# Kernel tuning notes

Hardware: AMD Instinct MI355X
Metric: run time of the kernel (lower is better)

Reference implementation:

```python
import jax, jax.numpy as jnp
import numpy as np

B = 2
T = 1024
D_MODEL = 1024
EXPAND = 2
D_INNER = D_MODEL * EXPAND  # 2048
D_STATE = 16
D_CONV = 4
DT_RANK = 64  # ceil(1024/16)


def setup_inputs() -> dict:
    key = jax.random.key(0)
    ks = jax.random.split(key, 9)
    s = 0.02
    x = jax.random.normal(ks[0], (B, T, D_MODEL), jnp.float32)
    in_proj_w = jax.random.normal(ks[1], (2 * D_INNER, D_MODEL), jnp.float32) * s
    conv_w = jax.random.normal(ks[2], (D_INNER, 1, D_CONV), jnp.float32) * 0.1
    conv_b = jax.random.normal(ks[3], (D_INNER,), jnp.float32) * 0.01
    x_proj_w = jax.random.normal(ks[4], (DT_RANK + 2 * D_STATE, D_INNER), jnp.float32) * s
    dt_proj_w = jax.random.normal(ks[5], (D_INNER, DT_RANK), jnp.float32) * s
    dt_proj_b = jax.random.uniform(ks[6], (D_INNER,), jnp.float32, -4.0, -2.0)
    A_log = jnp.log(jnp.tile(jnp.arange(1, D_STATE + 1, dtype=jnp.float32), (D_INNER, 1)))
    D_param = jnp.ones((D_INNER,), jnp.float32)
    out_proj_w = jax.random.normal(ks[7], (D_MODEL, D_INNER), jnp.float32) * s
    return {"x": x, "in_proj_w": in_proj_w, "conv_w": conv_w, "conv_b": conv_b,
            "x_proj_w": x_proj_w, "dt_proj_w": dt_proj_w, "dt_proj_b": dt_proj_b,
            "A_log": A_log, "D_param": D_param, "out_proj_w": out_proj_w}


def reference(x, in_proj_w, conv_w, conv_b, x_proj_w, dt_proj_w, dt_proj_b,
              A_log, D_param, out_proj_w):
    Bsz, Tlen, _ = x.shape
    # input projection -> (B,T,2*d_inner); split into x-branch and gate z
    xz = jnp.einsum('btd,ed->bte', x, in_proj_w)
    xs, z = jnp.split(xz, 2, axis=-1)
    # causal depthwise conv1d: torch pads both sides by d_conv-1 then slices [:T],
    # equivalent to left-pad d_conv-1
    xc = jnp.swapaxes(xs, 1, 2)  # (B, d_inner, T)
    xc = jax.lax.conv_general_dilated(xc, conv_w, window_strides=(1,),
                                      padding=[(D_CONV - 1, 0)],
                                      feature_group_count=D_INNER)
    xc = xc + conv_b[None, :, None]
    xs = jax.nn.silu(jnp.swapaxes(xc, 1, 2))  # (B,T,d_inner)
    A = -jnp.exp(A_log)  # (d_inner, d_state)
    x_dbl = jnp.einsum('bti,ei->bte', xs, x_proj_w)
    dt, Bv, Cv = jnp.split(x_dbl, [DT_RANK, DT_RANK + D_STATE], axis=-1)
    dt = jax.nn.softplus(jnp.einsum('btr,ir->bti', dt, dt_proj_w) + dt_proj_b)
    # selective scan: h_t = exp(dt_t*A)*h_{t-1} + (dt_t*x_t)*B_t ; y_t = <h_t, C_t>
    def step(h, inp):
        dt_t, B_t, C_t, x_t = inp  # (B,Di),(B,Ds),(B,Ds),(B,Di)
        dA = jnp.exp(dt_t[:, :, None] * A[None])        # (B,Di,Ds)
        h = dA * h + (dt_t * x_t)[:, :, None] * B_t[:, None, :]
        y_t = jnp.einsum('bds,bs->bd', h, C_t)
        return h, y_t
    tm = lambda a: jnp.swapaxes(a, 0, 1)  # time-major
    h0 = jnp.zeros((Bsz, D_INNER, D_STATE), x.dtype)
    _, ys = jax.lax.scan(step, h0, (tm(dt), tm(Bv), tm(Cv), tm(xs)))
    y = jnp.swapaxes(ys, 0, 1) + xs * D_param  # (B,T,d_inner)
    y = y * jax.nn.silu(z)
    return jnp.einsum('bti,di->btd', y, out_proj_w)
```

## Files before the change

kernel.cpp:

```cpp
#include <hip/hip_runtime.h>
#include <hip/hip_bf16.h>
#include <math.h>

#define B_SZ 2
#define T_LEN 1024
#define DMODEL 1024
#define DINNER 2048
#define DSTATE 16
#define DCONV 4
#define DTRANK 64
#define MTOK (B_SZ * T_LEN)

#define NC 32
#define CLEN (T_LEN / NC)
#define NCH (B_SZ * DINNER)
#define NSTATES (NCH * DSTATE)

#define XPK 8
#define XPKC (DINNER / XPK)

typedef __bf16 bf16x4 __attribute__((ext_vector_type(4)));
typedef __bf16 bf16x8 __attribute__((ext_vector_type(8)));
typedef float  f32x4  __attribute__((ext_vector_type(4)));

__device__ __forceinline__ float sigmoid_f(float v) { return 1.f / (1.f + __expf(-v)); }

__global__ __launch_bounds__(256) void convert4(const float* __restrict__ x,
                                                const float* __restrict__ w_in,
                                                const float* __restrict__ w_out,
                                                const float* __restrict__ w_xp,
                                                __bf16* __restrict__ xb,
                                                __bf16* __restrict__ wb_in,
                                                __bf16* __restrict__ wb_out,
                                                __bf16* __restrict__ wxp,
                                                float* __restrict__ xdbl)
{
    const int gi = blockIdx.x * blockDim.x + threadIdx.x;
    if (gi >= 1073152) {
        const int o = gi - 1073152;
        float4 z = make_float4(0.f, 0.f, 0.f, 0.f);
        reinterpret_cast<float4*>(xdbl)[2 * o]     = z;
        reinterpret_cast<float4*>(xdbl)[2 * o + 1] = z;
        return;
    }
    const float* src; __bf16* dst; int o;
    if (gi < 262144)       { src = x;     dst = xb;     o = gi; }
    else if (gi < 786432)  { src = w_in;  dst = wb_in;  o = gi - 262144; }
    else if (gi < 1048576) { src = w_out; dst = wb_out; o = gi - 786432; }
    else                   { src = w_xp;  dst = wxp;    o = gi - 1048576; }
    float4 a = reinterpret_cast<const float4*>(src)[2 * o];
    float4 b = reinterpret_cast<const float4*>(src)[2 * o + 1];
    bf16x8 v = {(__bf16)a.x, (__bf16)a.y, (__bf16)a.z, (__bf16)a.w,
                (__bf16)b.x, (__bf16)b.y, (__bf16)b.z, (__bf16)b.w};
    reinterpret_cast<bf16x8*>(dst)[o] = v;
}

template<int BN, typename CT>
__global__ __launch_bounds__(256) void mfma_gemm_bf16(const __bf16* __restrict__ A, int lda,
                                                      const __bf16* __restrict__ Bm, int ldb,
                                                      CT* __restrict__ C, int ldc, int K)
{
    constexpr int NF = BN / 32;
    constexpr int BCALLS = BN / 32;
    __shared__ __align__(16) __bf16 As[128 * 64];
    __shared__ __align__(16) __bf16 Bs[BN * 64];
    const int tid  = threadIdx.x;
    const int lane = tid & 63;
    const int w    = tid >> 6;
    const int wr   = w >> 1, wc = w & 1;
    const int m0   = blockIdx.y * 128, n0 = blockIdx.x * BN;

    f32x4 acc[4][NF];
    #pragma unroll
    for (int i = 0; i < 4; ++i)
        #pragma unroll
        for (int j = 0; j < NF; ++j) {
            f32x4 z = {0.f, 0.f, 0.f, 0.f};
            acc[i][j] = z;
        }

    const int fr = lane & 15;
    const int kq = (lane >> 4) * 8;

    for (int k0 = 0; k0 < K; k0 += 64) {
        #pragma unroll
        for (int c = 0; c < 4; ++c) {
            const int idx = c * 256 + tid;
            const int row = idx >> 3;
            const int kc  = (idx & 7) * 8;
            __builtin_amdgcn_global_load_lds(
                (const __attribute__((address_space(1))) unsigned int*)(A + (size_t)(m0 + row) * lda + k0 + kc),
                (__attribute__((address_space(3))) unsigned int*)(As + idx * 8),
                16, 0, 0);
        }
        #pragma unroll
        for (int c = 0; c < BCALLS; ++c) {
            const int idx = c * 256 + tid;
            const int row = idx >> 3;
            const int kc  = (idx & 7) * 8;
            __builtin_amdgcn_global_load_lds(
                (const __attribute__((address_space(1))) unsigned int*)(Bm + (size_t)(n0 + row) * ldb + k0 + kc),
                (__attribute__((address_space(3))) unsigned int*)(Bs + idx * 8),
                16, 0, 0);
        }
        __syncthreads();

        bf16x8 af[4][2], bfr[NF][2];
        #pragma unroll
        for (int i = 0; i < 4; ++i) {
            const __bf16* pa = As + (wr * 64 + i * 16 + fr) * 64 + kq;
            af[i][0] = *reinterpret_cast<const bf16x8*>(pa);
            af[i][1] = *reinterpret_cast<const bf16x8*>(pa + 32);
        }
        #pragma unroll
        for (int j = 0; j < NF; ++j) {
            const __bf16* pb = Bs + (wc * (BN / 2) + j * 16 + fr) * 64 + kq;
            bfr[j][0] = *reinterpret_cast<const bf16x8*>(pb);
            bfr[j][1] = *reinterpret_cast<const bf16x8*>(pb + 32);
        }
        #pragma unroll
        for (int i = 0; i < 4; ++i)
            #pragma unroll
            for (int j = 0; j < NF; ++j) {
                acc[i][j] = __builtin_amdgcn_mfma_f32_16x16x32_bf16(af[i][0], bfr[j][0], acc[i][j], 0, 0, 0);
                acc[i][j] = __builtin_amdgcn_mfma_f32_16x16x32_bf16(af[i][1], bfr[j][1], acc[i][j], 0, 0, 0);
            }
        __syncthreads();
    }

    const int crow = (lane >> 4) * 4;
    const int ccol = lane & 15;
    #pragma unroll
    for (int i = 0; i < 4; ++i)
        #pragma unroll
        for (int j = 0; j < NF; ++j) {
            CT* cp = C + (size_t)(m0 + wr * 64 + i * 16 + crow) * ldc
                       + n0 + wc * (BN / 2) + j * 16 + ccol;
            cp[0 * (size_t)ldc] = (CT)acc[i][j][0];
            cp[1 * (size_t)ldc] = (CT)acc[i][j][1];
            cp[2 * (size_t)ldc] = (CT)acc[i][j][2];
            cp[3 * (size_t)ldc] = (CT)acc[i][j][3];
        }
}

__global__ __launch_bounds__(256) void mfma_xproj(const __bf16* __restrict__ A,
                                                  const __bf16* __restrict__ Bm,
                                                  float* __restrict__ xdbl)
{
    __shared__ __align__(16) __bf16 As[128 * 64];
    __shared__ __align__(16) __bf16 Bs[32 * 64];
    const int tid  = threadIdx.x;
    const int lane = tid & 63;
    const int w    = tid >> 6;
    const int wr   = w >> 1, wc = w & 1;
    const int m0   = blockIdx.y * 128, n0 = blockIdx.x * 32;
    const int kbeg = blockIdx.z * XPKC;

    f32x4 acc[4];
    #pragma unroll
    for (int i = 0; i < 4; ++i) { f32x4 z = {0.f, 0.f, 0.f, 0.f}; acc[i] = z; }

    const int fr = lane & 15;
    const int kq = (lane >> 4) * 8;

    for (int k0 = kbeg; k0 < kbeg + XPKC; k0 += 64) {
        #pragma unroll
        for (int c = 0; c < 4; ++c) {
            const int idx = c * 256 + tid;
            const int row = idx >> 3;
            const int kc  = (idx & 7) * 8;
            __builtin_amdgcn_global_load_lds(
                (const __attribute__((address_space(1))) unsigned int*)(A + (size_t)(m0 + row) * DINNER + k0 + kc),
                (__attribute__((address_space(3))) unsigned int*)(As + idx * 8),
                16, 0, 0);
        }
        {
            const int row = tid >> 3;
            const int kc  = (tid & 7) * 8;
            __builtin_amdgcn_global_load_lds(
                (const __attribute__((address_space(1))) unsigned int*)(Bm + (size_t)(n0 + row) * DINNER + k0 + kc),
                (__attribute__((address_space(3))) unsigned int*)(Bs + tid * 8),
                16, 0, 0);
        }
        __syncthreads();

        bf16x8 af[4][2], bfr[2];
        #pragma unroll
        for (int i = 0; i < 4; ++i) {
            const __bf16* pa = As + (wr * 64 + i * 16 + fr) * 64 + kq;
            af[i][0] = *reinterpret_cast<const bf16x8*>(pa);
            af[i][1] = *reinterpret_cast<const bf16x8*>(pa + 32);
        }
        {
            const __bf16* pb = Bs + (wc * 16 + fr) * 64 + kq;
            bfr[0] = *reinterpret_cast<const bf16x8*>(pb);
            bfr[1] = *reinterpret_cast<const bf16x8*>(pb + 32);
        }
        #pragma unroll
        for (int i = 0; i < 4; ++i) {
            acc[i] = __builtin_amdgcn_mfma_f32_16x16x32_bf16(af[i][0], bfr[0], acc[i], 0, 0, 0);
            acc[i] = __builtin_amdgcn_mfma_f32_16x16x32_bf16(af[i][1], bfr[1], acc[i], 0, 0, 0);
        }
        __syncthreads();
    }

    const int crow = (lane >> 4) * 4;
    const int ccol = lane & 15;
    const int n = n0 + wc * 16 + ccol;
    #pragma unroll
    for (int i = 0; i < 4; ++i) {
        const int m = m0 + wr * 64 + i * 16 + crow;
        unsafeAtomicAdd(&xdbl[(size_t)(m + 0) * 96 + n], acc[i][0]);
        unsafeAtomicAdd(&xdbl[(size_t)(m + 1) * 96 + n], acc[i][1]);
        unsafeAtomicAdd(&xdbl[(size_t)(m + 2) * 96 + n], acc[i][2]);
        unsafeAtomicAdd(&xdbl[(size_t)(m + 3) * 96 + n], acc[i][3]);
    }
}

__global__ __launch_bounds__(256) void mfma_dtproj(const float* __restrict__ xdbl,
                                                   const float* __restrict__ dtw,
                                                   const float* __restrict__ dtbias,
                                                   __bf16* __restrict__ dtb)
{
    __shared__ __align__(16) __bf16 As0[128 * 64];
    __shared__ __align__(16) __bf16 Bs0[128 * 64];
    const int tid  = threadIdx.x;
    const int lane = tid & 63;
    const int w    = tid >> 6;
    const int wr   = w >> 1, wc = w & 1;
    const int m0 = (blockIdx.x >> 4) * 128;
    const int n0 = (blockIdx.x & 15) * 128;

    #pragma unroll
    for (int c = 0; c < 8; ++c) {
        const int idx = c * 256 + tid;
        const int row = idx >> 4;
        const int c4  = (idx & 15) * 4;
        float4 va = *reinterpret_cast<const float4*>(&xdbl[(size_t)(m0 + row) * 96 + c4]);
        bf16x4 ba = {(__bf16)va.x, (__bf16)va.y, (__bf16)va.z, (__bf16)va.w};
        *reinterpret_cast<bf16x4*>(&As0[row * 64 + c4]) = ba;
        float4 vb = *reinterpret_cast<const float4*>(&dtw[(size_t)(n0 + row) * DTRANK + c4]);
        bf16x4 bb = {(__bf16)vb.x, (__bf16)vb.y, (__bf16)vb.z, (__bf16)vb.w};
        *reinterpret_cast<bf16x4*>(&Bs0[row * 64 + c4]) = bb;
    }
    __syncthreads();

    const int fr = lane & 15;
    const int kq = (lane >> 4) * 8;
    f32x4 acc[4][4];
    #pragma unroll
    for (int i = 0; i < 4; ++i)
        #pragma unroll
        for (int j = 0; j < 4; ++j) {
            f32x4 z = {0.f, 0.f, 0.f, 0.f};
            acc[i][j] = z;
        }
    bf16x8 af[4][2], bfr[4][2];
    #pragma unroll
    for (int i = 0; i < 4; ++i) {
        const __bf16* pa = As0 + (wr * 64 + i * 16 + fr) * 64 + kq;
        af[i][0] = *reinterpret_cast<const bf16x8*>(pa);
        af[i][1] = *reinterpret_cast<const bf16x8*>(pa + 32);
    }
    #pragma unroll
    for (int j = 0; j < 4; ++j) {
        const __bf16* pb = Bs0 + (wc * 64 + j * 16 + fr) * 64 + kq;
        bfr[j][0] = *reinterpret_cast<const bf16x8*>(pb);
        bfr[j][1] = *reinterpret_cast<const bf16x8*>(pb + 32);
    }
    #pragma unroll
    for (int i = 0; i < 4; ++i)
        #pragma unroll
        for (int j = 0; j < 4; ++j) {
            acc[i][j] = __builtin_amdgcn_mfma_f32_16x16x32_bf16(af[i][0], bfr[j][0], acc[i][j], 0, 0, 0);
            acc[i][j] = __builtin_amdgcn_mfma_f32_16x16x32_bf16(af[i][1], bfr[j][1], acc[i][j], 0, 0, 0);
        }

    const int crow = (lane >> 4) * 4;
    const int ccol = lane & 15;
    #pragma unroll
    for (int i = 0; i < 4; ++i)
        #pragma unroll
        for (int j = 0; j < 4; ++j) {
            const int m = m0 + wr * 64 + i * 16 + crow;
            const int n = n0 + wc * 64 + j * 16 + ccol;
            const float bn = dtbias[n];
            #pragma unroll
            for (int r = 0; r < 4; ++r) {
                float v = acc[i][j][r] + bn;
                v = (v > 20.f) ? v : log1pf(__expf(v));
                dtb[(size_t)(m + r) * DINNER + n] = (__bf16)v;
            }
        }
}

__global__ __launch_bounds__(256) void conv_silu_v8(const __bf16* __restrict__ xzb,
                                                    const float* __restrict__ cw,
                                                    const float* __restrict__ cb,
                                                    __bf16* __restrict__ xsb)
{
    const int gid = blockIdx.x * blockDim.x + threadIdx.x;
    const int dg  = gid & (DINNER / 8 - 1);
    const int m   = gid >> 8;
    const int t   = m & (T_LEN - 1);
    const int d0  = dg * 8;

    float acc[8];
    {
        float4 b0 = *reinterpret_cast<const float4*>(&cb[d0]);
        float4 b1 = *reinterpret_cast<const float4*>(&cb[d0 + 4]);
        acc[0] = b0.x; acc[1] = b0.y; acc[2] = b0.z; acc[3] = b0.w;
        acc[4] = b1.x; acc[5] = b1.y; acc[6] = b1.z; acc[7] = b1.w;
    }
    float4 wv[8];
    #pragma unroll
    for (int c = 0; c < 8; ++c)
        wv[c] = *reinterpret_cast<const float4*>(&cw[(d0 + c) * DCONV]);

    #pragma unroll
    for (int j = 0; j < DCONV; ++j) {
        const int tt = t - (DCONV - 1) + j;
        if (tt >= 0) {
            bf16x8 v = *reinterpret_cast<const bf16x8*>(
                &xzb[(size_t)(m - (DCONV - 1) + j) * (2 * DINNER) + d0]);
            acc[0] = fmaf((float)v[0], (&wv[0].x)[j], acc[0]);
            acc[1] = fmaf((float)v[1], (&wv[1].x)[j], acc[1]);
            acc[2] = fmaf((float)v[2], (&wv[2].x)[j], acc[2]);
            acc[3] = fmaf((float)v[3], (&wv[3].x)[j], acc[3]);
            acc[4] = fmaf((float)v[4], (&wv[4].x)[j], acc[4]);
            acc[5] = fmaf((float)v[5], (&wv[5].x)[j], acc[5]);
            acc[6] = fmaf((float)v[6], (&wv[6].x)[j], acc[6]);
            acc[7] = fmaf((float)v[7], (&wv[7].x)[j], acc[7]);
        }
    }
    bf16x8 o;
    #pragma unroll
    for (int c = 0; c < 8; ++c) {
        float s = acc[c] * sigmoid_f(acc[c]);
        o[c] = (__bf16)s;
    }
    *reinterpret_cast<bf16x8*>(&xsb[(size_t)m * DINNER + d0]) = o;
}

__global__ __launch_bounds__(256) void scan_pass1(const __bf16* __restrict__ dtb,
                                                  const __bf16* __restrict__ xsb,
                                                  const float* __restrict__ xdbl,
                                                  const float* __restrict__ A_log,
                                                  float* __restrict__ Pb,
                                                  float* __restrict__ Bb)
{
    __shared__ float sB[CLEN][16];
    const int tid = threadIdx.x;
    const int g   = blockIdx.x * 256 + tid;
    const int c   = blockIdx.y;
    const int b   = g >> 11;
    const int d   = g & (DINNER - 1);
    const int m0  = b * T_LEN + c * CLEN;

    if (tid < CLEN * 4) {
        int t = tid >> 2, s4 = (tid & 3) * 4;
        *reinterpret_cast<float4*>(&sB[t][s4]) =
            *reinterpret_cast<const float4*>(&xdbl[(size_t)(m0 + t) * 96 + DTRANK + s4]);
    }
    __syncthreads();

    float a[DSTATE], h[DSTATE];
    #pragma unroll
    for (int s4 = 0; s4 < DSTATE; s4 += 4) {
        float4 v = *reinterpret_cast<const float4*>(&A_log[d * DSTATE + s4]);
        a[s4 + 0] = -__expf(v.x); a[s4 + 1] = -__expf(v.y);
        a[s4 + 2] = -__expf(v.z); a[s4 + 3] = -__expf(v.w);
        h[s4 + 0] = 0.f; h[s4 + 1] = 0.f; h[s4 + 2] = 0.f; h[s4 + 3] = 0.f;
    }

    float sumdt = 0.f;
    float dtc = (float)dtb[(size_t)m0 * DINNER + d];
    float xc  = (float)xsb[(size_t)m0 * DINNER + d];
    for (int t = 0; t < CLEN; ++t) {
        float dtn = 0.f, xn = 0.f;
        if (t + 1 < CLEN) {
            dtn = (float)dtb[(size_t)(m0 + t + 1) * DINNER + d];
            xn  = (float)xsb[(size_t)(m0 + t + 1) * DINNER + d];
        }
        sumdt += dtc;
        const float u = dtc * xc;
        #pragma unroll
        for (int s = 0; s < DSTATE; ++s) {
            const float dA = __expf(dtc * a[s]);
            h[s] = fmaf(dA, h[s], u * sB[t][s]);
        }
        dtc = dtn; xc = xn;
    }

    float* pp = Pb + ((size_t)c * NCH + g) * DSTATE;
    float* bp = Bb + ((size_t)c * NCH + g) * DSTATE;
    #pragma unroll
    for (int s4 = 0; s4 < DSTATE; s4 += 4) {
        float4 pv = {__expf(a[s4] * sumdt), __expf(a[s4 + 1] * sumdt),
                     __expf(a[s4 + 2] * sumdt), __expf(a[s4 + 3] * sumdt)};
        *reinterpret_cast<float4*>(pp + s4) = pv;
        float4 hv = {h[s4], h[s4 + 1], h[s4 + 2], h[s4 + 3]};
        *reinterpret_cast<float4*>(bp + s4) = hv;
    }
}

__global__ __launch_bounds__(256) void scan_pass2(const float* __restrict__ Pb,
                                                  float* __restrict__ Bb)
{
    const int idx = blockIdx.x * blockDim.x + threadIdx.x;
    float h = 0.f;
    #pragma unroll
    for (int c = 0; c < NC; ++c) {
        const size_t o = (size_t)c * NSTATES + idx;
        const float P  = Pb[o];
        const float Bv = Bb[o];
        Bb[o] = h;
        h = fmaf(P, h, Bv);
    }
}

__global__ __launch_bounds__(256) void scan_pass3(const __bf16* __restrict__ dtb,
                                                  const __bf16* __restrict__ xsb,
                                                  const float* __restrict__ xdbl,
                                                  const float* __restrict__ Hs,
                                                  const float* __restrict__ A_log,
                                                  const float* __restrict__ Dp,
                                                  const __bf16* __restrict__ xzb,
                                                  __bf16* __restrict__ yMb)
{
    __shared__ float sBC[CLEN][32];
    const int tid = threadIdx.x;
    const int g   = blockIdx.x * 256 + tid;
    const int c   = blockIdx.y;
    const int b   = g >> 11;
    const int d   = g & (DINNER - 1);
    const int m0  = b * T_LEN + c * CLEN;

    {
        int t = tid >> 3, col = (tid & 7) * 4;
        if (t < CLEN)
            *reinterpret_cast<float4*>(&sBC[t][col]) =
                *reinterpret_cast<const float4*>(&xdbl[(size_t)(m0 + t) * 96 + DTRANK + col]);
    }
    __syncthreads();

    float a[DSTATE], h[DSTATE];
    #pragma unroll
    for (int s4 = 0; s4 < DSTATE; s4 += 4) {
        float4 v = *reinterpret_cast<const float4*>(&A_log[d * DSTATE + s4]);
        a[s4 + 0] = -__expf(v.x); a[s4 + 1] = -__expf(v.y);
        a[s4 + 2] = -__expf(v.z); a[s4 + 3] = -__expf(v.w);
        float4 hv = *reinterpret_cast<const float4*>(
            Hs + ((size_t)c * NCH + g) * DSTATE + s4);
        h[s4 + 0] = hv.x; h[s4 + 1] = hv.y; h[s4 + 2] = hv.z; h[s4 + 3] = hv.w;
    }
    const float Dv = Dp[d];

    float dtc = (float)dtb[(size_t)m0 * DINNER + d];
    float xc  = (float)xsb[(size_t)m0 * DINNER + d];
    float zc  = (float)xzb[(size_t)m0 * (2 * DINNER) + DINNER + d];
    for (int t = 0; t < CLEN; ++t) {
        float dtn = 0.f, xn = 0.f, zn = 0.f;
        if (t + 1 < CLEN) {
            dtn = (float)dtb[(size_t)(m0 + t + 1) * DINNER + d];
            xn  = (float)xsb[(size_t)(m0 + t + 1) * DINNER + d];
            zn  = (float)xzb[(size_t)(m0 + t + 1) * (2 * DINNER) + DINNER + d];
        }
        const float u = dtc * xc;
        float y0 = 0.f, y1 = 0.f, y2 = 0.f, y3 = 0.f;
        #pragma unroll
        for (int s = 0; s < DSTATE; s += 4) {
            float dA0 = __expf(dtc * a[s + 0]);
            float dA1 = __expf(dtc * a[s + 1]);
            float dA2 = __expf(dtc * a[s + 2]);
            float dA3 = __expf(dtc * a[s + 3]);
            h[s + 0] = fmaf(dA0, h[s + 0], u * sBC[t][s + 0]);
            h[s + 1] = fmaf(dA1, h[s + 1], u * sBC[t][s + 1]);
            h[s + 2] = fmaf(dA2, h[s + 2], u * sBC[t][s + 2]);
            h[s + 3] = fmaf(dA3, h[s + 3], u * sBC[t][s + 3]);
            y0 = fmaf(h[s + 0], sBC[t][16 + s + 0], y0);
            y1 = fmaf(h[s + 1], sBC[t][16 + s + 1], y1);
            y2 = fmaf(h[s + 2], sBC[t][16 + s + 2], y2);
            y3 = fmaf(h[s + 3], sBC[t][16 + s + 3], y3);
        }
        float y = (y0 + y1) + (y2 + y3) + xc * Dv;
        const float gate = zc * sigmoid_f(zc);
        yMb[(size_t)(m0 + t) * DINNER + d] = (__bf16)(y * gate);
        dtc = dtn; xc = xn; zc = zn;
    }
}

extern "C" void kernel_launch(void* const* d_in, const int* in_sizes, int n_in,
                              void* d_out, int out_size, void* d_ws, size_t ws_size,
                              hipStream_t stream) {
    const float* x         = (const float*)d_in[0];
    const float* in_proj_w = (const float*)d_in[1];
    const float* conv_w    = (const float*)d_in[2];
    const float* conv_b    = (const float*)d_in[3];
    const float* x_proj_w  = (const float*)d_in[4];
    const float* dt_proj_w = (const float*)d_in[5];
    const float* dt_proj_b = (const float*)d_in[6];
    const float* A_log     = (const float*)d_in[7];
    const float* D_param   = (const float*)d_in[8];
    const float* out_proj_w= (const float*)d_in[9];
    float* out = (float*)d_out;

    float* ws = (float*)d_ws;
    const size_t M1 = (size_t)1024 * 1024;
    __bf16* xzb    = (__bf16*)ws;
    __bf16* xb     = (__bf16*)(ws + 4 * M1);
    __bf16* wb_in  = (__bf16*)(ws + 5 * M1);
    __bf16* wb_out = (__bf16*)(ws + 7 * M1);
    __bf16* wxp    = (__bf16*)(ws + 8 * M1);
    __bf16* xsb    = (__bf16*)(ws + 9 * M1);
    __bf16* dtb    = (__bf16*)(ws + 11 * M1);
    float*  xdbl   = ws + 13 * M1;
    float*  Pb     = ws + 14 * M1;
    float*  Bb     = ws + 16 * M1;
    __bf16* yMb    = (__bf16*)(ws + 18 * M1);

    dim3 blk(256);

    convert4<<<dim3(4288), blk, 0, stream>>>(x, in_proj_w, out_proj_w, x_proj_w,
                                             xb, wb_in, wb_out, wxp, xdbl);

    mfma_gemm_bf16<128, __bf16><<<dim3((2 * DINNER) / 128, MTOK / 128), blk, 0, stream>>>(
        xb, DMODEL, wb_in, DMODEL, xzb, 2 * DINNER, DMODEL);

    conv_silu_v8<<<dim3(MTOK * DINNER / 8 / 256), blk, 0, stream>>>(xzb, conv_w, conv_b, xsb);

    mfma_xproj<<<dim3(3, MTOK / 128, XPK), blk, 0, stream>>>(xsb, wxp, xdbl);

    mfma_dtproj<<<dim3(256), blk, 0, stream>>>(xdbl, dt_proj_w, dt_proj_b, dtb);

    scan_pass1<<<dim3(NCH / 256, NC), blk, 0, stream>>>(dtb, xsb, xdbl, A_log, Pb, Bb);
    scan_pass2<<<dim3(NSTATES / 256), blk, 0, stream>>>(Pb, Bb);
    scan_pass3<<<dim3(NCH / 256, NC), blk, 0, stream>>>(dtb, xsb, xdbl, Bb, A_log, D_param, xzb, yMb);

    mfma_gemm_bf16<64, float><<<dim3(DMODEL / 64, MTOK / 128), blk, 0, stream>>>(
        yMb, DINNER, wb_out, DINNER, out, DMODEL, DINNER);
}
```

Measured before the change: 180.4 us.

## Fuse three scan passes into one kernel with software grid barriers

Merges the chunked scan's three kernels into a single persistent kernel of 512 blocks that synchronise through atomic-counter grid barriers. The counter is zeroed by one extra thread range in the convert kernel. Keeping the B/C tile and A values on chip across phases removes two launch gaps and one reload of A. The barrier relies on all 512 blocks being co-resident and spins on global atomics, so it risks deadlock or added spin cost if occupancy assumptions fail.

```diff
diff --git a/kernel.cpp b/kernel.cpp
--- a/kernel.cpp
+++ b/kernel.cpp
@@ -15,6 +15,7 @@
 #define CLEN (T_LEN / NC)
 #define NCH (B_SZ * DINNER)
 #define NSTATES (NCH * DSTATE)
+#define SCAN_NBLK 512
 
 #define XPK 8
 #define XPKC (DINNER / XPK)
@@ -36,6 +37,7 @@
                                                 float* __restrict__ xdbl)
 {
     const int gi = blockIdx.x * blockDim.x + threadIdx.x;
+    if (gi >= 1097729) return;
     if (gi >= 1073152) {
         const int o = gi - 1073152;
         float4 z = make_float4(0.f, 0.f, 0.f, 0.f);
@@ -342,25 +344,42 @@
     *reinterpret_cast<bf16x8*>(&xsb[(size_t)m * DINNER + d0]) = o;
 }
 
-__global__ __launch_bounds__(256) void scan_pass1(const __bf16* __restrict__ dtb,
-                                                  const __bf16* __restrict__ xsb,
-                                                  const float* __restrict__ xdbl,
-                                                  const float* __restrict__ A_log,
-                                                  float* __restrict__ Pb,
-                                                  float* __restrict__ Bb)
+__device__ __forceinline__ void grid_barrier(int* cnt, int k) {
+    __syncthreads();
+    __threadfence();
+    if (threadIdx.x == 0) {
+        atomicAdd(&cnt[k], 1);
+        while (atomicAdd(&cnt[k], 0) < SCAN_NBLK) {}
+    }
+    __syncthreads();
+    __threadfence();
+}
+
+__global__ __launch_bounds__(256) void scan_fused3(const __bf16* __restrict__ dtb,
+                                                   const __bf16* __restrict__ xsb,
+                                                   const float* __restrict__ xdbl,
+                                                   const float* __restrict__ A_log,
+                                                   const float* __restrict__ Dp,
+                                                   const __bf16* __restrict__ xzb,
+                                                   float* __restrict__ Pb,
+                                                   float* __restrict__ Bb,
+                                                   __bf16* __restrict__ yMb,
+                                                   int* cnt)
 {
-    __shared__ float sB[CLEN][16];
+    __shared__ float sBC[CLEN][32];
     const int tid = threadIdx.x;
-    const int g   = blockIdx.x * 256 + tid;
-    const int c   = blockIdx.y;
+    const int bid = blockIdx.x;
+    const int cb  = bid & 15;
+    const int c   = bid >> 4;
+    const int g   = cb * 256 + tid;
     const int b   = g >> 11;
     const int d   = g & (DINNER - 1);
     const int m0  = b * T_LEN + c * CLEN;
 
-    if (tid < CLEN * 4) {
-        int t = tid >> 2, s4 = (tid & 3) * 4;
-        *reinterpret_cast<float4*>(&sB[t][s4]) =
-            *reinterpret_cast<const float4*>(&xdbl[(size_t)(m0 + t) * 96 + DTRANK + s4]);
+    {
+        const int t = tid >> 3, col = (tid & 7) * 4;
+        *reinterpret_cast<float4*>(&sBC[t][col]) =
+            *reinterpret_cast<const float4*>(&xdbl[(size_t)(m0 + t) * 96 + DTRANK + col]);
     }
     __syncthreads();
 
@@ -373,120 +392,92 @@
         h[s4 + 0] = 0.f; h[s4 + 1] = 0.f; h[s4 + 2] = 0.f; h[s4 + 3] = 0.f;
     }
 
-    float sumdt = 0.f;
-    float dtc = (float)dtb[(size_t)m0 * DINNER + d];
-    float xc  = (float)xsb[(size_t)m0 * DINNER + d];
-    for (int t = 0; t < CLEN; ++t) {
-        float dtn = 0.f, xn = 0.f;
-        if (t + 1 < CLEN) {
-            dtn = (float)dtb[(size_t)(m0 + t + 1) * DINNER + d];
-            xn  = (float)xsb[(size_t)(m0 + t + 1) * DINNER + d];
-        }
-        sumdt += dtc;
-        const float u = dtc * xc;
-        #pragma unroll
-        for (int s = 0; s < DSTATE; ++s) {
-            const float dA = __expf(dtc * a[s]);
-            h[s] = fmaf(dA, h[s], u * sB[t][s]);
-        }
-        dtc = dtn; xc = xn;
-    }
-
-    float* pp = Pb + ((size_t)c * NCH + g) * DSTATE;
-    float* bp = Bb + ((size_t)c * NCH + g) * DSTATE;
-    #pragma unroll
-    for (int s4 = 0; s4 < DSTATE; s4 += 4) {
-        float4 pv = {__expf(a[s4] * sumdt), __expf(a[s4 + 1] * sumdt),
-                     __expf(a[s4 + 2] * sumdt), __expf(a[s4 + 3] * sumdt)};
-        *reinterpret_cast<float4*>(pp + s4) = pv;
-        float4 hv = {h[s4], h[s4 + 1], h[s4 + 2], h[s4 + 3]};
-        *reinterpret_cast<float4*>(bp + s4) = hv;
-    }
-}
-
-__global__ __launch_bounds__(256) void scan_pass2(const float* __restrict__ Pb,
-                                                  float* __restrict__ Bb)
-{
-    const int idx = blockIdx.x * blockDim.x + threadIdx.x;
-    float h = 0.f;
-    #pragma unroll
-    for (int c = 0; c < NC; ++c) {
-        const size_t o = (size_t)c * NSTATES + idx;
-        const float P  = Pb[o];
-        const float Bv = Bb[o];
-        Bb[o] = h;
-        h = fmaf(P, h, Bv);
-    }
-}
-
-__global__ __launch_bounds__(256) void scan_pass3(const __bf16* __restrict__ dtb,
-                                                  const __bf16* __restrict__ xsb,
-                                                  const float* __restrict__ xdbl,
-                                                  const float* __restrict__ Hs,
-                                                  const float* __restrict__ A_log,
-                                                  const float* __restrict__ Dp,
-                                                  const __bf16* __restrict__ xzb,
-                                                  __bf16* __restrict__ yMb)
-{
-    __shared__ float sBC[CLEN][32];
-    const int tid = threadIdx.x;
-    const int g   = blockIdx.x * 256 + tid;
-    const int c   = blockIdx.y;
-    const int b   = g >> 11;
-    const int d   = g & (DINNER - 1);
-    const int m0  = b * T_LEN + c * CLEN;
-
     {
-        int t = tid >> 3, col = (tid & 7) * 4;
-        if (t < CLEN)
-            *reinterpret_cast<float4*>(&sBC[t][col]) =
-                *reinterpret_cast<const float4*>(&xdbl[(size_t)(m0 + t) * 96 + DTRANK + col]);
-    }
-    __syncthreads();
-
-    float a[DSTATE], h[DSTATE];
-    #pragma unroll
-    for (int s4 = 0; s4 < DSTATE; s4 += 4) {
-        float4 v = *reinterpret_cast<const float4*>(&A_log[d * DSTATE + s4]);
-        a[s4 + 0] = -__expf(v.x); a[s4 + 1] = -__expf(v.y);
-        a[s4 + 2] = -__expf(v.z); a[s4 + 3] = -__expf(v.w);
-        float4 hv = *reinterpret_cast<const float4*>(
-            Hs + ((size_t)c * NCH + g) * DSTATE + s4);
-        h[s4 + 0] = hv.x; h[s4 + 1] = hv.y; h[s4 + 2] = hv.z; h[s4 + 3] = hv.w;
-    }
-    const float Dv = Dp[d];
-
-    float dtc = (float)dtb[(size_t)m0 * DINNER + d];
-    float xc  = (float)xsb[(size_t)m0 * DINNER + d];
-    float zc  = (float)xzb[(size_t)m0 * (2 * DINNER) + DINNER + d];
-    for (int t = 0; t < CLEN; ++t) {
-        float dtn = 0.f, xn = 0.f, zn = 0.f;
-        if (t + 1 < CLEN) {
-            dtn = (float)dtb[(size_t)(m0 + t + 1) * DINNER + d];
-            xn  = (float)xsb[(size_t)(m0 + t + 1) * DINNER + d];
-            zn  = (float)xzb[(size_t)(m0 + t + 1) * (2 * DINNER) + DINNER + d];
-        }
-        const float u = dtc * xc;
-        float y0 = 0.f, y1 = 0.f, y2 = 0.f, y3 = 0.f;
-        #pragma unroll
-        for (int s = 0; s < DSTATE; s += 4) {
-            float dA0 = __expf(dtc * a[s + 0]);
-            float dA1 = __expf(dtc * a[s + 1]);
-            float dA2 = __expf(dtc * a[s + 2]);
-            float dA3 = __expf(dtc * a[s + 3]);
-            h[s + 0] = fmaf(dA0, h[s + 0], u * sBC[t][s + 0]);
-            h[s + 1] = fmaf(dA1, h[s + 1], u * sBC[t][s + 1]);
-            h[s + 2] = fmaf(dA2, h[s + 2], u * sBC[t][s + 2]);
-            h[s + 3] = fmaf(dA3, h[s + 3], u * sBC[t][s + 3]);
-            y0 = fmaf(h[s + 0], sBC[t][16 + s + 0], y0);
-            y1 = fmaf(h[s + 1], sBC[t][16 + s + 1], y1);
-            y2 = fmaf(h[s + 2], sBC[t][16 + s + 2], y2);
-            y3 = fmaf(h[s + 3], sBC[t][16 + s + 3], y3);
-        }
-        float y = (y0 + y1) + (y2 + y3) + xc * Dv;
-        const float gate = zc * sigmoid_f(zc);
-        yMb[(size_t)(m0 + t) * DINNER + d] = (__bf16)(y * gate);
-        dtc = dtn; xc = xn; zc = zn;
+        float sumdt = 0.f;
+        float dtc = (float)dtb[(size_t)m0 * DINNER + d];
+        float xc  = (float)xsb[(size_t)m0 * DINNER + d];
+        for (int t = 0; t < CLEN; ++t) {
+            float dtn = 0.f, xn = 0.f;
+            if (t + 1 < CLEN) {
+                dtn = (float)dtb[(size_t)(m0 + t + 1) * DINNER + d];
+                xn  = (float)xsb[(size_t)(m0 + t + 1) * DINNER + d];
+            }
+            sumdt += dtc;
+            const float u = dtc * xc;
+            #pragma unroll
+            for (int s = 0; s < DSTATE; ++s) {
+                const float dA = __expf(dtc * a[s]);
+                h[s] = fmaf(dA, h[s], u * sBC[t][s]);
+            }
+            dtc = dtn; xc = xn;
+        }
+        float* pp = Pb + ((size_t)c * NCH + g) * DSTATE;
+        float* bp = Bb + ((size_t)c * NCH + g) * DSTATE;
+        #pragma unroll
+        for (int s4 = 0; s4 < DSTATE; s4 += 4) {
+            float4 pv = {__expf(a[s4] * sumdt), __expf(a[s4 + 1] * sumdt),
+                         __expf(a[s4 + 2] * sumdt), __expf(a[s4 + 3] * sumdt)};
+            *reinterpret_cast<float4*>(pp + s4) = pv;
+            float4 hv = {h[s4], h[s4 + 1], h[s4 + 2], h[s4 + 3]};
+            *reinterpret_cast<float4*>(bp + s4) = hv;
+        }
+    }
+    grid_barrier(cnt, 0);
+
+    if (tid < 128) {
+        const int gt = bid * 128 + tid;
+        float hh = 0.f;
+        #pragma unroll
+        for (int cc = 0; cc < NC; ++cc) {
+            const size_t o = (size_t)cc * NSTATES + gt;
+            const float P  = Pb[o];
+            const float Bv = Bb[o];
+            Bb[o] = hh;
+            hh = fmaf(P, hh, Bv);
+        }
+    }
+    grid_barrier(cnt, 1);
+
+    {
+        const float* hp = Bb + ((size_t)c * NCH + g) * DSTATE;
+        #pragma unroll
+        for (int s4 = 0; s4 < DSTATE; s4 += 4) {
+            float4 hv = *reinterpret_cast<const float4*>(hp + s4);
+            h[s4 + 0] = hv.x; h[s4 + 1] = hv.y; h[s4 + 2] = hv.z; h[s4 + 3] = hv.w;
+        }
+        const float Dv = Dp[d];
+        float dtc = (float)dtb[(size_t)m0 * DINNER + d];
+        float xc  = (float)xsb[(size_t)m0 * DINNER + d];
+        float zc  = (float)xzb[(size_t)m0 * (2 * DINNER) + DINNER + d];
+        for (int t = 0; t < CLEN; ++t) {
+            float dtn = 0.f, xn = 0.f, zn = 0.f;
+            if (t + 1 < CLEN) {
+                dtn = (float)dtb[(size_t)(m0 + t + 1) * DINNER + d];
+                xn  = (float)xsb[(size_t)(m0 + t + 1) * DINNER + d];
+                zn  = (float)xzb[(size_t)(m0 + t + 1) * (2 * DINNER) + DINNER + d];
+            }
+            const float u = dtc * xc;
+            float y0 = 0.f, y1 = 0.f, y2 = 0.f, y3 = 0.f;
+            #pragma unroll
+            for (int s = 0; s < DSTATE; s += 4) {
+                float dA0 = __expf(dtc * a[s + 0]);
+                float dA1 = __expf(dtc * a[s + 1]);
+                float dA2 = __expf(dtc * a[s + 2]);
+                float dA3 = __expf(dtc * a[s + 3]);
+                h[s + 0] = fmaf(dA0, h[s + 0], u * sBC[t][s + 0]);
+                h[s + 1] = fmaf(dA1, h[s + 1], u * sBC[t][s + 1]);
+                h[s + 2] = fmaf(dA2, h[s + 2], u * sBC[t][s + 2]);
+                h[s + 3] = fmaf(dA3, h[s + 3], u * sBC[t][s + 3]);
+                y0 = fmaf(h[s + 0], sBC[t][16 + s + 0], y0);
+                y1 = fmaf(h[s + 1], sBC[t][16 + s + 1], y1);
+                y2 = fmaf(h[s + 2], sBC[t][16 + s + 2], y2);
+                y3 = fmaf(h[s + 3], sBC[t][16 + s + 3], y3);
+            }
+            float y = (y0 + y1) + (y2 + y3) + xc * Dv;
+            const float gate = zc * sigmoid_f(zc);
+            yMb[(size_t)(m0 + t) * DINNER + d] = (__bf16)(y * gate);
+            dtc = dtn; xc = xn; zc = zn;
+        }
     }
 }
 
@@ -515,13 +506,14 @@
     __bf16* xsb    = (__bf16*)(ws + 9 * M1);
     __bf16* dtb    = (__bf16*)(ws + 11 * M1);
     float*  xdbl   = ws + 13 * M1;
+    int*    cnt    = (int*)(xdbl + (size_t)MTOK * 96);
     float*  Pb     = ws + 14 * M1;
     float*  Bb     = ws + 16 * M1;
     __bf16* yMb    = (__bf16*)(ws + 18 * M1);
 
     dim3 blk(256);
 
-    convert4<<<dim3(4288), blk, 0, stream>>>(x, in_proj_w, out_proj_w, x_proj_w,
+    convert4<<<dim3(4289), blk, 0, stream>>>(x, in_proj_w, out_proj_w, x_proj_w,
                                              xb, wb_in, wb_out, wxp, xdbl);
 
     mfma_gemm_bf16<128, __bf16><<<dim3((2 * DINNER) / 128, MTOK / 128), blk, 0, stream>>>(
@@ -533,9 +525,8 @@
 
     mfma_dtproj<<<dim3(256), blk, 0, stream>>>(xdbl, dt_proj_w, dt_proj_b, dtb);
 
-    scan_pass1<<<dim3(NCH / 256, NC), blk, 0, stream>>>(dtb, xsb, xdbl, A_log, Pb, Bb);
-    scan_pass2<<<dim3(NSTATES / 256), blk, 0, stream>>>(Pb, Bb);
-    scan_pass3<<<dim3(NCH / 256, NC), blk, 0, stream>>>(dtb, xsb, xdbl, Bb, A_log, D_param, xzb, yMb);
+    scan_fused3<<<dim3(SCAN_NBLK), blk, 0, stream>>>(dtb, xsb, xdbl, A_log, D_param,
+                                                     xzb, Pb, Bb, yMb, cnt);
 
     mfma_gemm_bf16<64, float><<<dim3(DMODEL / 64, MTOK / 128), blk, 0, stream>>>(
         yMb, DINNER, wb_out, DINNER, out, DMODEL, DINNER);
```

Result: slower. 403.9 us (+123.9%).
